# Kernel tuning notes

Measured on AMD Instinct MI355X. Metric: run time of the kernel, lower is better.

The kernel has to match this reference:

```python
import jax, jax.numpy as jnp
import numpy as np

B, C_IN, H, W = 4, 2048, 64, 64
C_INTER = C_IN // 4          # 512
C_QK = C_INTER // 8          # 64
C_OUT = 512


def conv3x3(x, w):
    # x: [B,C,H,W], w: [O,I,3,3], padding=1, no bias
    return jax.lax.conv_general_dilated(
        x, w, window_strides=(1, 1), padding=((1, 1), (1, 1)),
        dimension_numbers=('NCHW', 'OIHW', 'NCHW'))


def criss_cross_attention(x, qw, kw, vw, gamma):
    # x: [B,Ci,H,W]; qw,kw: [Cqk,Ci]; vw: [Ci,Ci]; gamma: scalar
    b, c, h, w = x.shape
    q = jnp.einsum('bchw,oc->bohw', x, qw)
    k = jnp.einsum('bchw,oc->bohw', x, kw)
    v = jnp.einsum('bchw,oc->bohw', x, vw)
    # column (H-axis) affinity with -inf diagonal to avoid double self-count
    eH = jnp.einsum('bchw,bciw->bhwi', q, k)                  # [B,H,W,H]
    diag = jnp.eye(h, dtype=bool)[None, :, None, :]           # [1,H,1,H]
    eH = jnp.where(diag, -jnp.inf, eH)
    # row (W-axis) affinity
    eW = jnp.einsum('bchw,bchj->bhwj', q, k)                  # [B,H,W,W]
    att = jax.nn.softmax(jnp.concatenate([eH, eW], axis=-1), axis=-1)
    attH, attW = att[..., :h], att[..., h:]
    outH = jnp.einsum('bhwi,bciw->bchw', attH, v)
    outW = jnp.einsum('bhwj,bchj->bchw', attW, v)
    return gamma * (outH + outW) + x


def setup_inputs() -> dict:
    key = jax.random.key(0)
    ks = jax.random.split(key, 8)
    s = 0.02
    return {
        'x': jax.random.normal(ks[0], (B, C_IN, H, W), jnp.float32),
        'conva_w': jax.random.normal(ks[1], (C_INTER, C_IN, 3, 3), jnp.float32) * s,
        'q_w': jax.random.normal(ks[2], (C_QK, C_INTER), jnp.float32) * s,
        'k_w': jax.random.normal(ks[3], (C_QK, C_INTER), jnp.float32) * s,
        'v_w': jax.random.normal(ks[4], (C_INTER, C_INTER), jnp.float32) * s,
        'gamma': jax.random.normal(ks[5], (), jnp.float32) * 0.1,
        'convb_w': jax.random.normal(ks[6], (C_INTER, C_INTER, 3, 3), jnp.float32) * s,
        'bottleneck_w': jax.random.normal(ks[7], (C_OUT, C_IN + C_INTER, 3, 3), jnp.float32) * s,
        'recurrence': 2,
    }


def reference(x, conva_w, q_w, k_w, v_w, gamma, convb_w, bottleneck_w, recurrence):
    out = conv3x3(x, conva_w)
    for _ in range(recurrence):
        out = criss_cross_attention(out, q_w, k_w, v_w, gamma)
    out = conv3x3(out, convb_w)
    out = conv3x3(jnp.concatenate([x, out], axis=1), bottleneck_w)
    return out
```

## Files before the change

kernel.cpp:

```cpp
#include <hip/hip_runtime.h>
#include <hip/hip_bf16.h>
#include <stdint.h>

typedef unsigned short u16;
typedef __bf16 bf16x8 __attribute__((ext_vector_type(8)));
typedef float f32x4 __attribute__((ext_vector_type(4)));

#define DEVINL __device__ __forceinline__

DEVINL float bf2f(u16 v) {
    union { uint32_t u; float f; } c; c.u = ((uint32_t)v) << 16; return c.f;
}
DEVINL u16 f2bf(float f) {
    union { float f; uint32_t u; } c; c.f = f;
    uint32_t x = c.u;
    x += 0x7fffu + ((x >> 16) & 1u);
    return (u16)(x >> 16);
}

DEVINL void load_lds16(const u16* g, char* lds_uniform_base) {
    __builtin_amdgcn_global_load_lds(
        (const __attribute__((address_space(1))) void*)g,
        (__attribute__((address_space(3))) void*)lds_uniform_base,
        16, 0, 0);
}

template<int OM>
__launch_bounds__(256)
__global__ void conv_gemm(const u16* __restrict__ in, int IH, int IW, int inC, int cofs,
                          int K, int ntaps, const u16* __restrict__ wt, int N,
                          void* __restrict__ outp, int outC, int nwg)
{
    __shared__ __align__(16) u16 ldsA[2][8192];
    __shared__ __align__(16) u16 ldsB[2][8192];

    const int id  = blockIdx.x;
    const int swz = (id & 7) * (nwg >> 3) + (id >> 3);
    const int m0 = (swz & 127) << 7;
    const int n0 = (swz >> 7) << 7;

    const int tid  = threadIdx.x;
    const int lane = tid & 63;
    const int wv   = tid >> 6;
    const int l7 = lane & 7, l3 = lane >> 3;
    const int g  = lane >> 4;
    const int cOff = (l7 ^ l3) << 3;

    const int wn = (wv & 1) * 64;
    const int wm = (wv >> 1) * 64;

    f32x4 acc[4][4];
#pragma unroll
    for (int i = 0; i < 4; ++i)
#pragma unroll
        for (int j = 0; j < 4; ++j) acc[i][j] = (f32x4){0.f, 0.f, 0.f, 0.f};

    const u16* aBase = wt + (size_t)(n0 + wv * 32 + l3) * K + cOff;
    const u16* bBase[4];
#pragma unroll
    for (int q = 0; q < 4; ++q) {
        int mA = m0 + wv * 32 + q * 8 + l3;
        int bb = mA >> 12, yy = (mA >> 6) & 63, xx = mA & 63;
        bBase[q] = in + ((size_t)(bb * IH + yy) * IW + xx) * inC + cofs + cOff;
    }

    const int kpt = K >> 6;
    const int nsteps = ntaps * kpt;
    int s_tap = 0, s_k0 = 0;
    size_t s_wofs = 0;
    int s_xofs = 0;

    auto STAGE = [&](int buf) {
        char* la = (char*)ldsA[buf] + wv * 4096;
        char* lb = (char*)ldsB[buf] + wv * 4096;
        const u16* wp = aBase + s_wofs;
        const int xo = s_xofs;
#pragma unroll
        for (int q = 0; q < 4; ++q) {
            load_lds16(wp + (size_t)(q * 8) * K, la + q * 1024);
            load_lds16(bBase[q] + xo,            lb + q * 1024);
        }
    };
    auto ADV = [&]() {
        ++s_tap;
        if (s_tap == ntaps) { s_tap = 0; s_k0 += 64; }
        int ty = s_tap / 3, tx = s_tap % 3;
        s_wofs = (size_t)s_tap * N * K + s_k0;
        s_xofs = (ty * IW + tx) * inC + s_k0;
    };

    STAGE(0); ADV();
    int cur = 0;
    const int rb = (lane & 15) << 7;

    for (int s = 0; s < nsteps; ++s) {
        __syncthreads();
        if (s + 1 < nsteps) { STAGE(cur ^ 1); ADV(); }

        const char* laW = (const char*)ldsA[cur] + (wn << 7);
        const char* lbW = (const char*)ldsB[cur] + (wm << 7);
#pragma unroll
        for (int kk = 0; kk < 2; ++kk) {
            const int ca = (((kk << 2) + g) ^ l7) << 4;
            bf16x8 af[4], bfr[4];
#pragma unroll
            for (int f = 0; f < 4; ++f) {
                af[f]  = *(const bf16x8*)(laW + (f << 11) + rb + ca);
                bfr[f] = *(const bf16x8*)(lbW + (f << 11) + rb + ca);
            }
#pragma unroll
            for (int fn = 0; fn < 4; ++fn)
#pragma unroll
                for (int fm = 0; fm < 4; ++fm)
                    acc[fn][fm] = __builtin_amdgcn_mfma_f32_16x16x32_bf16(
                        af[fn], bfr[fm], acc[fn][fm], 0, 0, 0);
        }
        cur ^= 1;
    }

    const int rn = (lane >> 4) * 4;
    const int cm = lane & 15;
#pragma unroll
    for (int fn = 0; fn < 4; ++fn) {
#pragma unroll
        for (int fm = 0; fm < 4; ++fm) {
            const int n = n0 + wn + fn * 16 + rn;
            const int m = m0 + wm + fm * 16 + cm;
            const int b = m >> 12, y = (m >> 6) & 63, x = m & 63;
            f32x4 v = acc[fn][fm];
            if constexpr (OM == 1) {
                ushort4 pk;
                pk.x = f2bf(v[0]); pk.y = f2bf(v[1]); pk.z = f2bf(v[2]); pk.w = f2bf(v[3]);
                *(ushort4*)((u16*)outp + (size_t)m * outC + n) = pk;
            } else if constexpr (OM == 2) {
                ushort4 pk;
                pk.x = f2bf(v[0]); pk.y = f2bf(v[1]); pk.z = f2bf(v[2]); pk.w = f2bf(v[3]);
                size_t o = ((size_t)(b * 66 + y + 1) * 66 + (x + 1)) * 2560 + 2048 + n;
                *(ushort4*)((u16*)outp + o) = pk;
            } else {
                float* op = (float*)outp;
#pragma unroll
                for (int r = 0; r < 4; ++r)
                    op[((size_t)(b * 512 + n + r) << 12) + (y << 6) + x] = v[r];
            }
        }
    }
}


__global__ void wtrans(const float* __restrict__ w, u16* __restrict__ wo, int O, int C)
{
    int idx = blockIdx.x * 256 + threadIdx.x;
    int total = O * C;
    if (idx >= total) return;
    const float* src = w + (size_t)idx * 9;
    float v[9];
#pragma unroll
    for (int t = 0; t < 9; ++t) v[t] = src[t];
#pragma unroll
    for (int t = 0; t < 9; ++t) wo[(size_t)t * total + idx] = f2bf(v[t]);
}

__global__ void wqkv_concat(const float* __restrict__ q, const float* __restrict__ k,
                            const float* __restrict__ v, u16* __restrict__ o)
{
    int idx = blockIdx.x * 256 + threadIdx.x;
    if (idx >= 640 * 512) return;
    int row = idx >> 9;
    float val = (row < 64) ? q[idx] : (row < 128) ? k[idx - 64 * 512] : v[idx - 128 * 512];
    o[idx] = f2bf(val);
}

__global__ void nchw_to_nhwc_pad(const float* __restrict__ x, u16* __restrict__ xp)
{
    size_t idx = (size_t)blockIdx.x * 256 + threadIdx.x;
    int m  = (int)(idx & 16383);
    int cc = (int)(idx >> 14);
    int xw = m & 63, y = (m >> 6) & 63, b = m >> 12;
    const float* xs = x + ((size_t)(b * 2048 + cc * 8)) * 4096 + (y << 6) + xw;
    union { u16 u[8]; uint4 v4; } tmp;
#pragma unroll
    for (int j = 0; j < 8; ++j) tmp.u[j] = f2bf(xs[(size_t)j * 4096]);
    u16* dst = xp + ((size_t)(b * 66 + y + 1) * 66 + (xw + 1)) * 2560 + cc * 8;
    *(uint4*)dst = tmp.v4;
}

__global__ void pad512(const u16* __restrict__ F, u16* __restrict__ FP)
{
    size_t idx = (size_t)blockIdx.x * 256 + threadIdx.x;
    int cc = (int)(idx & 63);
    int m  = (int)(idx >> 6);
    int xw = m & 63, y = (m >> 6) & 63, b = m >> 12;
    const uint4* src = (const uint4*)(F + (size_t)m * 512 + cc * 8);
    uint4* dst = (uint4*)(FP + ((size_t)(b * 66 + y + 1) * 66 + (xw + 1)) * 512 + cc * 8);
    *dst = *src;
}

__global__ void fill7777(float* __restrict__ o, int n)
{
    int idx = blockIdx.x * 256 + threadIdx.x;
    if (idx < n) o[idx] = 7777.0f;
}

#define NEGBIG -1.0e30f

__global__ void att_scoreH(const u16* __restrict__ QKV, float* __restrict__ ATT)
{
    const int bid = blockIdx.x;
    const int half = bid >> 8;
    const int b = (bid >> 6) & 3, x = bid & 63;
    __shared__ float q[32][65], kk[64][65];
    const int tid = threadIdx.x;
    for (int p = tid; p < 2048; p += 256) {
        int r = p >> 6, c = p & 63;
        size_t m = (size_t)((b << 12) + ((half * 32 + r) << 6) + x);
        q[r][c] = bf2f(QKV[m * 640 + c]);
    }
    for (int p = tid; p < 4096; p += 256) {
        int r = p >> 6, c = p & 63;
        size_t m = (size_t)((b << 12) + (r << 6) + x);
        kk[r][c] = bf2f(QKV[m * 640 + 64 + c]);
    }
    __syncthreads();
    for (int p = tid; p < 2048; p += 256) {
        int r = p >> 6, i = p & 63;
        float s = 0.f;
#pragma unroll 8
        for (int c = 0; c < 64; ++c) s += q[r][c] * kk[i][c];
        int y = half * 32 + r;
        if (i == y) s = NEGBIG;
        ATT[(size_t)((b << 12) + (y << 6) + x) * 128 + i] = s;
    }
}

__global__ void att_scoreW(const u16* __restrict__ QKV, float* __restrict__ ATT)
{
    const int bid = blockIdx.x;
    const int half = bid >> 8;
    const int b = (bid >> 6) & 3, y = bid & 63;
    const size_t mb = (size_t)((b << 12) + (y << 6));
    __shared__ float q[32][65], kk[64][65];
    const int tid = threadIdx.x;
    for (int p = tid; p < 2048; p += 256) {
        int r = p >> 6, c = p & 63;
        q[r][c] = bf2f(QKV[(mb + half * 32 + r) * 640 + c]);
    }
    for (int p = tid; p < 4096; p += 256) {
        int r = p >> 6, c = p & 63;
        kk[r][c] = bf2f(QKV[(mb + r) * 640 + 64 + c]);
    }
    __syncthreads();
    for (int p = tid; p < 2048; p += 256) {
        int r = p >> 6, j = p & 63;
        float s = 0.f;
#pragma unroll 8
        for (int c = 0; c < 64; ++c) s += q[r][c] * kk[j][c];
        ATT[(mb + half * 32 + r) * 128 + 64 + j] = s;
    }
}

__global__ void att_softmax(float* __restrict__ ATT)
{
    int wid = threadIdx.x >> 6, lane = threadIdx.x & 63;
    size_t pos = (size_t)blockIdx.x * 4 + wid;
    float* row = ATT + pos * 128;
    float a = row[lane], b = row[64 + lane];
    float mx = fmaxf(a, b);
    for (int o = 32; o; o >>= 1) mx = fmaxf(mx, __shfl_xor(mx, o));
    float ea = __expf(a - mx), eb = __expf(b - mx);
    float s = ea + eb;
    for (int o = 32; o; o >>= 1) s += __shfl_xor(s, o);
    float inv = 1.f / s;
    row[lane] = ea * inv;
    row[64 + lane] = eb * inv;
}

__launch_bounds__(256)
__global__ void att_outH(const u16* __restrict__ QKV, const float* __restrict__ ATT,
                         float* __restrict__ OH)
{
    const int bid = blockIdx.x;
    const int half = bid >> 8;
    const int b = (bid >> 6) & 3, x = bid & 63;
    __shared__ float A[32][65];
    const int tid = threadIdx.x;
    for (int p = tid; p < 2048; p += 256) {
        int r = p >> 6, i = p & 63;
        A[r][i] = ATT[(size_t)((b << 12) + ((half * 32 + r) << 6) + x) * 128 + i];
    }
    __syncthreads();
    const int wv = tid >> 6, lane = tid & 63;
    const int r0 = wv * 8;
    float acc[8][8];
#pragma unroll
    for (int cc = 0; cc < 8; ++cc)
#pragma unroll
        for (int yy = 0; yy < 8; ++yy) acc[cc][yy] = 0.f;
    for (int i = 0; i < 64; ++i) {
        float a[8];
#pragma unroll
        for (int yy = 0; yy < 8; ++yy) a[yy] = A[r0 + yy][i];
        const u16* vrow = QKV + (size_t)((b << 12) + (i << 6) + x) * 640 + 128;
#pragma unroll
        for (int cc = 0; cc < 8; ++cc) {
            float v = bf2f(vrow[cc * 64 + lane]);
#pragma unroll
            for (int yy = 0; yy < 8; ++yy) acc[cc][yy] += a[yy] * v;
        }
    }
    const int y0 = half * 32 + r0;
#pragma unroll
    for (int cc = 0; cc < 8; ++cc)
#pragma unroll
        for (int yy = 0; yy < 8; ++yy)
            OH[(size_t)((b << 12) + ((y0 + yy) << 6) + x) * 512 + cc * 64 + lane]
                = acc[cc][yy];
}

__launch_bounds__(256)
__global__ void att_outW_combine(const u16* __restrict__ QKV, const float* __restrict__ ATT,
                                 const float* __restrict__ OH, const u16* __restrict__ Fin,
                                 u16* __restrict__ Fout, const float* __restrict__ gamma)
{
    const int bid = blockIdx.x;
    const int half = bid >> 8;
    const int b = (bid >> 6) & 3, y = bid & 63;
    const size_t mb = (size_t)((b << 12) + (y << 6));
    __shared__ float A[32][65];
    const int tid = threadIdx.x;
    for (int p = tid; p < 2048; p += 256) {
        int r = p >> 6, j = p & 63;
        A[r][j] = ATT[(mb + half * 32 + r) * 128 + 64 + j];
    }
    const float g = gamma[0];
    __syncthreads();
    const int wv = tid >> 6, lane = tid & 63;
    const int r0 = wv * 8;
    float acc[8][8];
#pragma unroll
    for (int cc = 0; cc < 8; ++cc)
#pragma unroll
        for (int xx = 0; xx < 8; ++xx) acc[cc][xx] = 0.f;
    for (int j = 0; j < 64; ++j) {
        float a[8];
#pragma unroll
        for (int xx = 0; xx < 8; ++xx) a[xx] = A[r0 + xx][j];
        const u16* vrow = QKV + (mb + j) * 640 + 128;
#pragma unroll
        for (int cc = 0; cc < 8; ++cc) {
            float v = bf2f(vrow[cc * 64 + lane]);
#pragma unroll
            for (int xx = 0; xx < 8; ++xx) acc[cc][xx] += a[xx] * v;
        }
    }
    const int x0 = half * 32 + r0;
#pragma unroll
    for (int cc = 0; cc < 8; ++cc) {
#pragma unroll
        for (int xx = 0; xx < 8; ++xx) {
            size_t m = mb + x0 + xx;
            size_t o = m * 512 + cc * 64 + lane;
            Fout[o] = f2bf(g * (OH[o] + acc[cc][xx]) + bf2f(Fin[o]));
        }
    }
}

static constexpr size_t ALN = 512;
static inline size_t alup(size_t v) { return (v + ALN - 1) & ~(ALN - 1); }

extern "C" void kernel_launch(void* const* d_in, const int* in_sizes, int n_in,
                              void* d_out, int out_size, void* d_ws, size_t ws_size,
                              hipStream_t stream)
{
    (void)in_sizes; (void)n_in;
    const float* x       = (const float*)d_in[0];
    const float* conva_w = (const float*)d_in[1];
    const float* q_w     = (const float*)d_in[2];
    const float* k_w     = (const float*)d_in[3];
    const float* v_w     = (const float*)d_in[4];
    const float* gamma   = (const float*)d_in[5];
    const float* convb_w = (const float*)d_in[6];
    const float* bneck_w = (const float*)d_in[7];

    const size_t XP_B   = (size_t)4 * 66 * 66 * 2560 * 2;
    const size_t WB_B   = (size_t)9 * 512 * 512 * 2;
    const size_t WQKV_B = (size_t)640 * 512 * 2;
    const size_t F_B    = (size_t)4 * 4096 * 512 * 2;
    const size_t QKV_B  = (size_t)4 * 4096 * 640 * 2;
    const size_t ATT_B  = (size_t)4 * 4096 * 128 * 4;
    const size_t WA_B   = (size_t)9 * 512 * 2048 * 2;
    const size_t FP_B   = (size_t)4 * 66 * 66 * 512 * 2;
    const size_t WN_B   = (size_t)9 * 512 * 2560 * 2;

    size_t arena_B = alup(QKV_B) + alup(ATT_B);
    if (alup(FP_B) + alup(WN_B) > arena_B) arena_B = alup(FP_B) + alup(WN_B);
    if (alup(WA_B) > arena_B) arena_B = alup(WA_B);

    const size_t NEED = alup(XP_B) + alup(WB_B) + alup(WQKV_B) + 2 * alup(F_B) + arena_B;
    if (ws_size < NEED) {
        fill7777<<<(out_size + 255) / 256, 256, 0, stream>>>((float*)d_out, out_size);
        return;
    }

    char* p = (char*)d_ws;
    u16* XP   = (u16*)p; p += alup(XP_B);
    u16* WB   = (u16*)p; p += alup(WB_B);
    u16* WQKV = (u16*)p; p += alup(WQKV_B);
    u16* F0   = (u16*)p; p += alup(F_B);
    u16* F1   = (u16*)p; p += alup(F_B);
    char* arena = p;
    u16*   WA  = (u16*)arena;
    u16*   QKV = (u16*)arena;
    float* ATT = (float*)(arena + alup(QKV_B));
    u16*   FP  = (u16*)arena;
    u16*   WN  = (u16*)(arena + alup(FP_B));
    float* OH  = (float*)d_out;

    hipMemsetAsync(XP, 0, XP_B, stream);

    wtrans<<<(512 * 2048 + 255) / 256, 256, 0, stream>>>(conva_w, WA, 512, 2048);
    wtrans<<<(512 * 512 + 255) / 256, 256, 0, stream>>>(convb_w, WB, 512, 512);
    wqkv_concat<<<(640 * 512 + 255) / 256, 256, 0, stream>>>(q_w, k_w, v_w, WQKV);

    nchw_to_nhwc_pad<<<16384, 256, 0, stream>>>(x, XP);

    conv_gemm<1><<<512, 256, 0, stream>>>(XP, 66, 66, 2560, 0, 2048, 9,
                                          WA, 512, F0, 512, 512);

    const u16* Fi = F0;
    u16* Fo = F1;
    for (int it = 0; it < 2; ++it) {
        conv_gemm<1><<<640, 256, 0, stream>>>(Fi, 64, 64, 512, 0, 512, 1,
                                              WQKV, 640, QKV, 640, 640);
        att_scoreH<<<512, 256, 0, stream>>>(QKV, ATT);
        att_scoreW<<<512, 256, 0, stream>>>(QKV, ATT);
        att_softmax<<<4096, 256, 0, stream>>>(ATT);
        att_outH<<<512, 256, 0, stream>>>(QKV, ATT, OH);
        att_outW_combine<<<512, 256, 0, stream>>>(QKV, ATT, OH, Fi, Fo, gamma);
        const u16* t = Fi; Fi = Fo; Fo = (u16*)t;
    }

    hipMemsetAsync(FP, 0, FP_B, stream);
    pad512<<<4096, 256, 0, stream>>>(Fi, FP);
    wtrans<<<(512 * 2560 + 255) / 256, 256, 0, stream>>>(bneck_w, WN, 512, 2560);

    conv_gemm<2><<<512, 256, 0, stream>>>(FP, 66, 66, 512, 0, 512, 9,
                                          WB, 512, XP, 2560, 512);

    conv_gemm<3><<<512, 256, 0, stream>>>(XP, 66, 66, 2560, 0, 2560, 9,
                                          WN, 512, d_out, 512, 512);
}
```

Baseline: 1.140 ms.

## Enlarge conv GEMM tile to 256x128 with 512 threads and triple-buffered LDS pipeline

The implicit-GEMM conv kernel now runs 512-thread workgroups, each covering a 256-pixel by 128-channel output tile, so every weight tile loaded into LDS is reused across twice as many pixels. The LDS pipeline goes from double to triple buffering, with explicit vmcnt waits and barriers, so global-to-LDS loads run two steps ahead. Fragments are read from LDS before the buffer is refilled, which separates memory traffic from the MFMA loop. The larger LDS footprint (about 144 KB) and the 512-thread launch bounds limit occupancy, and the hand-written waitcnt logic is fragile.

```diff
diff --git a/kernel.cpp b/kernel.cpp
--- a/kernel.cpp
+++ b/kernel.cpp
@@ -26,18 +26,18 @@
 }
 
 template<int OM>
-__launch_bounds__(256)
+__launch_bounds__(512, 2)
 __global__ void conv_gemm(const u16* __restrict__ in, int IH, int IW, int inC, int cofs,
                           int K, int ntaps, const u16* __restrict__ wt, int N,
                           void* __restrict__ outp, int outC, int nwg)
 {
-    __shared__ __align__(16) u16 ldsA[2][8192];
-    __shared__ __align__(16) u16 ldsB[2][8192];
+    __shared__ __align__(16) u16 ldsA[3][8192];
+    __shared__ __align__(16) u16 ldsB[3][16384];
 
     const int id  = blockIdx.x;
     const int swz = (id & 7) * (nwg >> 3) + (id >> 3);
-    const int m0 = (swz & 127) << 7;
-    const int n0 = (swz >> 7) << 7;
+    const int m0 = (swz & 63) << 8;
+    const int n0 = (swz >> 6) << 7;
 
     const int tid  = threadIdx.x;
     const int lane = tid & 63;
@@ -55,13 +55,16 @@
 #pragma unroll
         for (int j = 0; j < 4; ++j) acc[i][j] = (f32x4){0.f, 0.f, 0.f, 0.f};
 
-    const u16* aBase = wt + (size_t)(n0 + wv * 32 + l3) * K + cOff;
-    const u16* bBase[4];
-#pragma unroll
-    for (int q = 0; q < 4; ++q) {
-        int mA = m0 + wv * 32 + q * 8 + l3;
+    const u16* aB[2];
+#pragma unroll
+    for (int j = 0; j < 2; ++j)
+        aB[j] = wt + (size_t)(n0 + wv * 16 + j * 8 + l3) * K + cOff;
+    const u16* bB[4];
+#pragma unroll
+    for (int j = 0; j < 4; ++j) {
+        int mA = m0 + wv * 32 + j * 8 + l3;
         int bb = mA >> 12, yy = (mA >> 6) & 63, xx = mA & 63;
-        bBase[q] = in + ((size_t)(bb * IH + yy) * IW + xx) * inC + cofs + cOff;
+        bB[j] = in + ((size_t)(bb * IH + yy) * IW + xx) * inC + cofs + cOff;
     }
 
     const int kpt = K >> 6;
@@ -71,15 +74,16 @@
     int s_xofs = 0;
 
     auto STAGE = [&](int buf) {
-        char* la = (char*)ldsA[buf] + wv * 4096;
+        char* la = (char*)ldsA[buf] + wv * 2048;
         char* lb = (char*)ldsB[buf] + wv * 4096;
-        const u16* wp = aBase + s_wofs;
+        const u16* wp0 = aB[0] + s_wofs;
+        const u16* wp1 = aB[1] + s_wofs;
         const int xo = s_xofs;
-#pragma unroll
-        for (int q = 0; q < 4; ++q) {
-            load_lds16(wp + (size_t)(q * 8) * K, la + q * 1024);
-            load_lds16(bBase[q] + xo,            lb + q * 1024);
-        }
+        load_lds16(wp0, la);
+        load_lds16(wp1, la + 1024);
+#pragma unroll
+        for (int j = 0; j < 4; ++j)
+            load_lds16(bB[j] + xo, lb + j * 1024);
     };
     auto ADV = [&]() {
         ++s_tap;
@@ -90,32 +94,46 @@
     };
 
     STAGE(0); ADV();
-    int cur = 0;
+    STAGE(1); ADV();
+    STAGE(2); ADV();
+
     const int rb = (lane & 15) << 7;
 
     for (int s = 0; s < nsteps; ++s) {
-        __syncthreads();
-        if (s + 1 < nsteps) { STAGE(cur ^ 1); ADV(); }
-
-        const char* laW = (const char*)ldsA[cur] + (wn << 7);
-        const char* lbW = (const char*)ldsB[cur] + (wm << 7);
+        if (s + 2 < nsteps)      asm volatile("s_waitcnt vmcnt(12)" ::: "memory");
+        else if (s + 1 < nsteps) asm volatile("s_waitcnt vmcnt(6)"  ::: "memory");
+        else                     asm volatile("s_waitcnt vmcnt(0)"  ::: "memory");
+        __builtin_amdgcn_s_barrier();
+        __builtin_amdgcn_sched_barrier(0);
+
+        const int buf = s % 3;
+        const char* laW = (const char*)ldsA[buf] + (wn << 7);
+        const char* lbW = (const char*)ldsB[buf] + (wm << 7);
+        bf16x8 af[2][4], bfr[2][4];
 #pragma unroll
         for (int kk = 0; kk < 2; ++kk) {
             const int ca = (((kk << 2) + g) ^ l7) << 4;
-            bf16x8 af[4], bfr[4];
 #pragma unroll
             for (int f = 0; f < 4; ++f) {
-                af[f]  = *(const bf16x8*)(laW + (f << 11) + rb + ca);
-                bfr[f] = *(const bf16x8*)(lbW + (f << 11) + rb + ca);
+                af[kk][f]  = *(const bf16x8*)(laW + (f << 11) + rb + ca);
+                bfr[kk][f] = *(const bf16x8*)(lbW + (f << 11) + rb + ca);
             }
+        }
+        asm volatile("s_waitcnt lgkmcnt(0)" ::: "memory");
+        __builtin_amdgcn_sched_barrier(0);
+        __builtin_amdgcn_s_barrier();
+        __builtin_amdgcn_sched_barrier(0);
+
+        if (s + 3 < nsteps) { STAGE(buf); ADV(); }
+
+#pragma unroll
+        for (int kk = 0; kk < 2; ++kk)
 #pragma unroll
             for (int fn = 0; fn < 4; ++fn)
 #pragma unroll
                 for (int fm = 0; fm < 4; ++fm)
                     acc[fn][fm] = __builtin_amdgcn_mfma_f32_16x16x32_bf16(
-                        af[fn], bfr[fm], acc[fn][fm], 0, 0, 0);
-        }
-        cur ^= 1;
+                        af[kk][fn], bfr[kk][fm], acc[fn][fm], 0, 0, 0);
     }
 
     const int rn = (lane >> 4) * 4;
@@ -424,14 +442,14 @@
 
     nchw_to_nhwc_pad<<<16384, 256, 0, stream>>>(x, XP);
 
-    conv_gemm<1><<<512, 256, 0, stream>>>(XP, 66, 66, 2560, 0, 2048, 9,
-                                          WA, 512, F0, 512, 512);
+    conv_gemm<1><<<256, 512, 0, stream>>>(XP, 66, 66, 2560, 0, 2048, 9,
+                                          WA, 512, F0, 512, 256);
 
     const u16* Fi = F0;
     u16* Fo = F1;
     for (int it = 0; it < 2; ++it) {
-        conv_gemm<1><<<640, 256, 0, stream>>>(Fi, 64, 64, 512, 0, 512, 1,
-                                              WQKV, 640, QKV, 640, 640);
+        conv_gemm<1><<<320, 512, 0, stream>>>(Fi, 64, 64, 512, 0, 512, 1,
+                                              WQKV, 640, QKV, 640, 320);
         att_scoreH<<<512, 256, 0, stream>>>(QKV, ATT);
         att_scoreW<<<512, 256, 0, stream>>>(QKV, ATT);
         att_softmax<<<4096, 256, 0, stream>>>(ATT);
@@ -444,9 +462,9 @@
     pad512<<<4096, 256, 0, stream>>>(Fi, FP);
     wtrans<<<(512 * 2560 + 255) / 256, 256, 0, stream>>>(bneck_w, WN, 512, 2560);
 
-    conv_gemm<2><<<512, 256, 0, stream>>>(FP, 66, 66, 512, 0, 512, 9,
-                                          WB, 512, XP, 2560, 512);
-
-    conv_gemm<3><<<512, 256, 0, stream>>>(XP, 66, 66, 2560, 0, 2560, 9,
-                                          WN, 512, d_out, 512, 512);
-}
+    conv_gemm<2><<<256, 512, 0, stream>>>(FP, 66, 66, 512, 0, 512, 9,
+                                          WB, 512, XP, 2560, 256);
+
+    conv_gemm<3><<<256, 512, 0, stream>>>(XP, 66, 66, 2560, 0, 2560, 9,
+                                          WN, 512, d_out, 512, 256);
+}
```

Result: no change. 1.161 ms (+1.8%).

## Fuse softmax into attention output kernels and zero only padding borders

Applied to the files above, without the earlier changes.

Drops the standalone softmax kernel. Each of the two attention-output kernels now loads the full 128-wide score row into LDS with vector loads and recomputes the softmax redundantly before using its half. The full-buffer memsets of the padded NHWC buffers are replaced by a kernel that zeroes only the one-pixel border cells, since the interior is overwritten anyway. This saves a write-back pass over the attention matrix and large memset traffic, at the cost of doubled softmax work and doubled score-row reads.

```diff
diff --git a/kernel.cpp b/kernel.cpp
--- a/kernel.cpp
+++ b/kernel.cpp
@@ -196,6 +196,24 @@
     *dst = *src;
 }
 
+__global__ void zero_border(u16* __restrict__ P, int C)
+{
+    int idx = blockIdx.x * 256 + threadIdx.x;
+    int cw = C >> 3;
+    int total = 4 * 260 * cw;
+    if (idx >= total) return;
+    int ch   = (idx % cw) * 8;
+    int cell = (idx / cw) % 260;
+    int b    = idx / (cw * 260);
+    int y, x;
+    if (cell < 66)       { y = 0;              x = cell;       }
+    else if (cell < 132) { y = 65;             x = cell - 66;  }
+    else if (cell < 196) { y = cell - 132 + 1; x = 0;          }
+    else                 { y = cell - 196 + 1; x = 65;         }
+    size_t o = ((size_t)(b * 66 + y) * 66 + x) * C + ch;
+    *(uint4*)(P + o) = (uint4){0, 0, 0, 0};
+}
+
 __global__ void fill7777(float* __restrict__ o, int n)
 {
     int idx = blockIdx.x * 256 + threadIdx.x;
@@ -259,20 +277,28 @@
     }
 }
 
-__global__ void att_softmax(float* __restrict__ ATT)
-{
-    int wid = threadIdx.x >> 6, lane = threadIdx.x & 63;
-    size_t pos = (size_t)blockIdx.x * 4 + wid;
-    float* row = ATT + pos * 128;
-    float a = row[lane], b = row[64 + lane];
-    float mx = fmaxf(a, b);
-    for (int o = 32; o; o >>= 1) mx = fmaxf(mx, __shfl_xor(mx, o));
-    float ea = __expf(a - mx), eb = __expf(b - mx);
-    float s = ea + eb;
-    for (int o = 32; o; o >>= 1) s += __shfl_xor(s, o);
-    float inv = 1.f / s;
-    row[lane] = ea * inv;
-    row[64 + lane] = eb * inv;
+DEVINL void softmax32(float (*A)[132], int tid)
+{
+    const int row = tid >> 3, sub = tid & 7;
+    float lm = -3.4e38f;
+#pragma unroll
+    for (int i = sub * 16; i < sub * 16 + 16; ++i) lm = fmaxf(lm, A[row][i]);
+    lm = fmaxf(lm, __shfl_xor(lm, 1));
+    lm = fmaxf(lm, __shfl_xor(lm, 2));
+    lm = fmaxf(lm, __shfl_xor(lm, 4));
+    float ls = 0.f;
+#pragma unroll
+    for (int i = sub * 16; i < sub * 16 + 16; ++i) {
+        float e = __expf(A[row][i] - lm);
+        A[row][i] = e;
+        ls += e;
+    }
+    ls += __shfl_xor(ls, 1);
+    ls += __shfl_xor(ls, 2);
+    ls += __shfl_xor(ls, 4);
+    float inv = 1.f / ls;
+#pragma unroll
+    for (int i = sub * 16; i < sub * 16 + 16; ++i) A[row][i] *= inv;
 }
 
 __launch_bounds__(256)
@@ -282,12 +308,15 @@
     const int bid = blockIdx.x;
     const int half = bid >> 8;
     const int b = (bid >> 6) & 3, x = bid & 63;
-    __shared__ float A[32][65];
+    __shared__ float A[32][132];
     const int tid = threadIdx.x;
-    for (int p = tid; p < 2048; p += 256) {
-        int r = p >> 6, i = p & 63;
-        A[r][i] = ATT[(size_t)((b << 12) + ((half * 32 + r) << 6) + x) * 128 + i];
-    }
+    for (int p = tid; p < 1024; p += 256) {
+        int r = p >> 5, q4 = p & 31;
+        *(f32x4*)&A[r][q4 * 4] = *(const f32x4*)
+            &ATT[(size_t)((b << 12) + ((half * 32 + r) << 6) + x) * 128 + q4 * 4];
+    }
+    __syncthreads();
+    softmax32(A, tid);
     __syncthreads();
     const int wv = tid >> 6, lane = tid & 63;
     const int r0 = wv * 8;
@@ -326,13 +355,16 @@
     const int half = bid >> 8;
     const int b = (bid >> 6) & 3, y = bid & 63;
     const size_t mb = (size_t)((b << 12) + (y << 6));
-    __shared__ float A[32][65];
+    __shared__ float A[32][132];
     const int tid = threadIdx.x;
-    for (int p = tid; p < 2048; p += 256) {
-        int r = p >> 6, j = p & 63;
-        A[r][j] = ATT[(mb + half * 32 + r) * 128 + 64 + j];
+    for (int p = tid; p < 1024; p += 256) {
+        int r = p >> 5, q4 = p & 31;
+        *(f32x4*)&A[r][q4 * 4] = *(const f32x4*)
+            &ATT[(mb + half * 32 + r) * 128 + q4 * 4];
     }
     const float g = gamma[0];
+    __syncthreads();
+    softmax32(A, tid);
     __syncthreads();
     const int wv = tid >> 6, lane = tid & 63;
     const int r0 = wv * 8;
@@ -344,7 +376,7 @@
     for (int j = 0; j < 64; ++j) {
         float a[8];
 #pragma unroll
-        for (int xx = 0; xx < 8; ++xx) a[xx] = A[r0 + xx][j];
+        for (int xx = 0; xx < 8; ++xx) a[xx] = A[r0 + xx][64 + j];
         const u16* vrow = QKV + (mb + j) * 640 + 128;
 #pragma unroll
         for (int cc = 0; cc < 8; ++cc) {
@@ -416,7 +448,7 @@
     u16*   WN  = (u16*)(arena + alup(FP_B));
     float* OH  = (float*)d_out;
 
-    hipMemsetAsync(XP, 0, XP_B, stream);
+    zero_border<<<(4 * 260 * (2560 / 8) + 255) / 256, 256, 0, stream>>>(XP, 2560);
 
     wtrans<<<(512 * 2048 + 255) / 256, 256, 0, stream>>>(conva_w, WA, 512, 2048);
     wtrans<<<(512 * 512 + 255) / 256, 256, 0, stream>>>(convb_w, WB, 512, 512);
@@ -434,13 +466,12 @@
                                               WQKV, 640, QKV, 640, 640);
         att_scoreH<<<512, 256, 0, stream>>>(QKV, ATT);
         att_scoreW<<<512, 256, 0, stream>>>(QKV, ATT);
-        att_softmax<<<4096, 256, 0, stream>>>(ATT);
         att_outH<<<512, 256, 0, stream>>>(QKV, ATT, OH);
         att_outW_combine<<<512, 256, 0, stream>>>(QKV, ATT, OH, Fi, Fo, gamma);
         const u16* t = Fi; Fi = Fo; Fo = (u16*)t;
     }
 
-    hipMemsetAsync(FP, 0, FP_B, stream);
+    zero_border<<<(4 * 260 * (512 / 8) + 255) / 256, 256, 0, stream>>>(FP, 512);
     pad512<<<4096, 256, 0, stream>>>(Fi, FP);
     wtrans<<<(512 * 2560 + 255) / 256, 256, 0, stream>>>(bneck_w, WN, 512, 2560);
 
```

New measurement: 1.114 ms. 2.3% less time.
